# Performance work log

Measured on AMD Instinct MI355X. Metric: run time of the kernel, lower is better.

## Reference

```python
import jax, jax.numpy as jnp
import numpy as np

D, M, N = 1024, 16, 16384
H = D // M  # head dim = 64
C = 10.0    # tanh logit clipping


def setup_inputs() -> dict:
    key = jax.random.key(0)
    kb, kq, km, k1, k2, k3, k4 = jax.random.split(key, 7)
    def xavier(k, shape):
        # torch xavier_uniform: fan_in = prod(shape[1:]), fan_out = shape[0]*prod(shape[2:])
        fan_in = int(np.prod(shape[1:]))
        fan_out = shape[0] * int(np.prod(shape[2:]))
        bound = float(np.sqrt(6.0 / (fan_in + fan_out)))
        return jax.random.uniform(k, shape, jnp.float32, -bound, bound)
    return {
        "b": jax.random.normal(kb, (N, D), jnp.float32),
        "q_s_bar": jax.random.normal(kq, (D,), jnp.float32),
        "mask": jax.random.randint(km, (N,), 0, 2).astype(bool),
        "W_k_bar": xavier(k1, (M, H, D)),
        "W_v_bar": xavier(k2, (M, H, D)),
        "W_k": xavier(k3, (D, D)),
        "W_q": xavier(k4, (D, D)),
    }


def reference(b, q_s_bar, mask, W_k_bar, W_v_bar, W_k, W_q):
    # k_bar, v_bar: (N, M, H)  == matmul(W, b.t()).permute(2,0,1)
    k_bar = jnp.einsum('mhd,nd->nmh', W_k_bar, b)
    v_bar = jnp.einsum('mhd,nd->nmh', W_v_bar, b)
    k = b @ W_k.T                      # (N, D) == matmul(W_k, b.t()).t()
    q = q_s_bar.reshape(M, H)          # (M, H)
    # c_bar: (N, M, M) == matmul(k_bar, q.T) / sqrt(h)
    c_bar = jnp.einsum('nmh,gh->nmg', k_bar, q) / np.float32(np.sqrt(H))
    scores = jnp.where(mask[:, None, None], c_bar, -jnp.inf)
    attn = jax.nn.softmax(scores, axis=0)          # softmax over N
    # (N,M,M) @ (N,M,H) batched -> (N,M,H); view(N,-1).sum(0) -> (D,)
    q_s = jnp.einsum('nmg,ngh->nmh', attn, v_bar).reshape(N, D).sum(0)
    c = (k @ (W_q @ q_s)) / np.float32(np.sqrt(D))  # (N,)
    c = C * jnp.tanh(c)
    return jnp.where(mask, c, -jnp.inf)
```

## Files before the change

### kernel.cpp

```cpp
#include <hip/hip_runtime.h>
#include <math.h>
#include <float.h>

#define NN 16384
#define DD 1024
#define MM 16
#define HH 64
#define MG 256

typedef __attribute__((ext_vector_type(8))) short bh8;
typedef __attribute__((ext_vector_type(4))) float f32x4;

__device__ inline float bf2f(unsigned short u) {
    union { unsigned int i; float f; } v;
    v.i = ((unsigned int)u) << 16;
    return v.f;
}

__device__ inline unsigned short f2bf(float f) {
    union { float f; unsigned int i; } v;
    v.f = f;
    unsigned int r = v.i + 0x7FFFu + ((v.i >> 16) & 1u);
    return (unsigned short)(r >> 16);
}

__device__ inline float ld1(const void* p, long i, int isf) {
    return isf ? ((const float*)p)[i] : bf2f(((const unsigned short*)p)[i]);
}

__device__ inline float4 ld4(const void* p, long i, int isf) {
    if (isf) return *(const float4*)((const float*)p + i);
    ushort4 u = *(const ushort4*)((const unsigned short*)p + i);
    return make_float4(bf2f(u.x), bf2f(u.y), bf2f(u.z), bf2f(u.w));
}

__device__ inline bool get_mask(const unsigned char* mp, int n, int flag) {
    return flag ? (mp[n] != 0) : (mp[4 * n] != 0);
}

__device__ inline void gl_lds16(const void* g, void* l) {
    __builtin_amdgcn_global_load_lds(
        (const __attribute__((address_space(1))) unsigned int*)g,
        (__attribute__((address_space(3))) unsigned int*)l, 16, 0, 0);
}

__global__ void detect(const unsigned char* __restrict__ mp,
                       const unsigned char* __restrict__ bb, int* flags,
                       float* __restrict__ u) {
    int i = blockIdx.x * 256 + threadIdx.x;
    if (i < DD) u[i] = 0.f;
    int v1 = ((i & 3) != 0 && mp[i] != 0) ? 1 : 0;
    unsigned char c = bb[4 * i + 1];
    bool expish = (c == 0x00) || (c == 0x80) || (c >= 0x30 && c <= 0x47) ||
                  (c >= 0xB0 && c <= 0xC7);
    int v2 = expish ? 0 : 1;
    unsigned long long b1 = __ballot(v1);
    unsigned long long b2 = __ballot(v2);
    if ((threadIdx.x & 63) == 0) {
        if (b1) atomicOr(&flags[0], 1);
        if (b2) atomicOr(&flags[1], 1);
    }
}

__global__ void fold_k(const void* __restrict__ Wkb, const void* __restrict__ qsb,
                       unsigned short* __restrict__ Abf, const int* __restrict__ flags) {
    __shared__ float q[DD];
    int isf = flags[1];
    int m = blockIdx.x;
    int d = blockIdx.y * 128 + threadIdx.x;
    for (int i = threadIdx.x; i < DD; i += 128) q[i] = ld1(qsb, i, isf);
    __syncthreads();
    float acc[MM];
#pragma unroll
    for (int g = 0; g < MM; g++) acc[g] = 0.f;
    for (int h = 0; h < HH; h++) {
        float w = ld1(Wkb, (long)(m * HH + h) * DD + d, isf);
#pragma unroll
        for (int g = 0; g < MM; g++) acc[g] += w * q[g * HH + h];
    }
#pragma unroll
    for (int g = 0; g < MM; g++)
        Abf[(long)(m * MM + g) * DD + d] = f2bf(acc[g] * 0.125f);
}

__global__ void cvt_b(const void* __restrict__ bB, unsigned short* __restrict__ bbf,
                      unsigned short* __restrict__ bT, const int* __restrict__ flags) {
    __shared__ unsigned short tl[64 * 72];
    int isf = flags[1];
    int bn = blockIdx.x, bd = blockIdx.y;
    int t = threadIdx.x;
    int i0 = t >> 4, jg = t & 15;
#pragma unroll
    for (int it = 0; it < 4; ++it) {
        int i = i0 + it * 16;
        long gidx = (long)(bn * 64 + i) * DD + bd * 64 + jg * 4;
        ushort4 o;
        if (isf) {
            float4 v = *(const float4*)((const float*)bB + gidx);
            o.x = f2bf(v.x); o.y = f2bf(v.y); o.z = f2bf(v.z); o.w = f2bf(v.w);
        } else {
            o = *(const ushort4*)((const unsigned short*)bB + gidx);
        }
        *(ushort4*)&bbf[gidx] = o;
        *(ushort4*)&tl[i * 72 + jg * 4] = o;
    }
    __syncthreads();
    int p = t >> 2, g = t & 3;
#pragma unroll
    for (int k = 0; k < 4; ++k) {
        int nl = g * 4 + k * 16;
        ushort4 o;
        o.x = tl[(nl + 0) * 72 + p];
        o.y = tl[(nl + 1) * 72 + p];
        o.z = tl[(nl + 2) * 72 + p];
        o.w = tl[(nl + 3) * 72 + p];
        *(ushort4*)&bT[(long)(bd * 64 + p) * NN + bn * 64 + nl] = o;
    }
}

__global__ __launch_bounds__(256) void gemm_b_mfma(
    const unsigned short* __restrict__ Abf, const unsigned short* __restrict__ bbf,
    const unsigned char* __restrict__ mp, const int* __restrict__ flags,
    unsigned short* __restrict__ Cb) {
    __shared__ __align__(16) unsigned short As[128 * 64];
    __shared__ __align__(16) unsigned short Bs[64 * 64];
    int m0 = blockIdx.x * 128, n0 = blockIdx.y * 64;
    int t = threadIdx.x;
    int lane = t & 63, w = t >> 6;
    int wm = w >> 1, wn = w & 1;
    int r = lane & 15, q = lane >> 4;
    f32x4 acc[4][2] = {};
    for (int k0 = 0; k0 < DD; k0 += 64) {
#pragma unroll
        for (int i = 0; i < 4; i++) {
            int L = (i * 4 + w) * 64 + lane;
            int row = L >> 3, c = (L & 7) ^ (row & 7);
            gl_lds16(&Abf[(long)(m0 + row) * DD + k0 + c * 8], &As[(i * 4 + w) * 512]);
        }
#pragma unroll
        for (int i = 0; i < 2; i++) {
            int L = (i * 4 + w) * 64 + lane;
            int row = L >> 3, c = (L & 7) ^ (row & 7);
            gl_lds16(&bbf[(long)(n0 + row) * DD + k0 + c * 8], &Bs[(i * 4 + w) * 512]);
        }
        __syncthreads();
#pragma unroll
        for (int h = 0; h < 2; h++) {
            bh8 af[4], bfr[2];
#pragma unroll
            for (int fi = 0; fi < 4; fi++) {
                int row = wm * 64 + fi * 16 + r;
                int ck = (h * 4 + q) ^ (row & 7);
                af[fi] = *(const bh8*)&As[row * 64 + ck * 8];
            }
#pragma unroll
            for (int fj = 0; fj < 2; fj++) {
                int row = wn * 32 + fj * 16 + r;
                int ck = (h * 4 + q) ^ (row & 7);
                bfr[fj] = *(const bh8*)&Bs[row * 64 + ck * 8];
            }
#pragma unroll
            for (int fi = 0; fi < 4; fi++)
#pragma unroll
                for (int fj = 0; fj < 2; fj++)
                    acc[fi][fj] = __builtin_amdgcn_mfma_f32_16x16x32_bf16(
                        af[fi], bfr[fj], acc[fi][fj], 0, 0, 0);
        }
        __syncthreads();
    }
    int mflag = flags[0];
#pragma unroll
    for (int fj = 0; fj < 2; fj++) {
        int gn = n0 + wn * 32 + fj * 16 + r;
        float nb = get_mask(mp, gn, mflag) ? 0.f : -INFINITY;
#pragma unroll
        for (int fi = 0; fi < 4; fi++)
#pragma unroll
            for (int reg = 0; reg < 4; reg++) {
                int gm = m0 + wm * 64 + fi * 16 + q * 4 + reg;
                Cb[(long)gm * NN + gn] = f2bf(acc[fi][fj][reg] + nb);
            }
    }
}

__global__ void softmax_part(const unsigned short* __restrict__ Cb,
                             float* __restrict__ sws) {
    __shared__ float red[256];
    int mg = blockIdx.x, z = blockIdx.y, t = threadIdx.x;
    bh8 v8 = *(const bh8*)&Cb[(long)mg * NN + z * 2048 + t * 8];
    float x[8];
#pragma unroll
    for (int j = 0; j < 8; j++) x[j] = bf2f((unsigned short)v8[j]);
    float mx = x[0];
#pragma unroll
    for (int j = 1; j < 8; j++) mx = fmaxf(mx, x[j]);
    red[t] = mx;
    __syncthreads();
    for (int s = 128; s; s >>= 1) {
        if (t < s) red[t] = fmaxf(red[t], red[t + s]);
        __syncthreads();
    }
    mx = red[0];
    __syncthreads();
    float sm = 0.f;
#pragma unroll
    for (int j = 0; j < 8; j++) sm += expf(x[j] - mx);
    red[t] = sm;
    __syncthreads();
    for (int s = 128; s; s >>= 1) {
        if (t < s) red[t] += red[t + s];
        __syncthreads();
    }
    if (t == 0) {
        sws[(mg * 8 + z) * 2] = mx;
        sws[(mg * 8 + z) * 2 + 1] = red[0];
    }
}

__global__ void softmax_norm(const unsigned short* __restrict__ Cb,
                             const float* __restrict__ sws,
                             unsigned short* __restrict__ P) {
    int mg = blockIdx.x, z = blockIdx.y, t = threadIdx.x;
    float mx = -INFINITY;
#pragma unroll
    for (int z2 = 0; z2 < 8; z2++) mx = fmaxf(mx, sws[(mg * 8 + z2) * 2]);
    float S = 0.f;
#pragma unroll
    for (int z2 = 0; z2 < 8; z2++) {
        float pm = sws[(mg * 8 + z2) * 2], ps = sws[(mg * 8 + z2) * 2 + 1];
        if (pm > -INFINITY) S += ps * expf(pm - mx);
    }
    float inv = 1.0f / S;
    long i = (long)mg * NN + z * 2048 + t * 8;
    bh8 v8 = *(const bh8*)&Cb[i];
    bh8 o;
#pragma unroll
    for (int j = 0; j < 8; j++)
        o[j] = (short)f2bf(expf(bf2f((unsigned short)v8[j]) - mx) * inv);
    *(bh8*)&P[i] = o;
}

__global__ __launch_bounds__(256) void gemm_d_mfma(
    const unsigned short* __restrict__ P, const unsigned short* __restrict__ bT,
    unsigned short* __restrict__ Tpart) {
    __shared__ __align__(16) unsigned short As[128 * 64];
    __shared__ __align__(16) unsigned short Bs[64 * 64];
    int m0 = blockIdx.x * 128, d0 = blockIdx.y * 64;
    long kbase = (long)blockIdx.z * 1024;
    unsigned short* Cg = Tpart + (long)blockIdx.z * (MG * DD);
    int t = threadIdx.x;
    int lane = t & 63, w = t >> 6;
    int wm = w >> 1, wn = w & 1;
    int r = lane & 15, q = lane >> 4;
    f32x4 acc[4][2] = {};
    for (int k0 = 0; k0 < 1024; k0 += 64) {
#pragma unroll
        for (int i = 0; i < 4; i++) {
            int L = (i * 4 + w) * 64 + lane;
            int row = L >> 3, c = (L & 7) ^ (row & 7);
            gl_lds16(&P[(long)(m0 + row) * NN + kbase + k0 + c * 8], &As[(i * 4 + w) * 512]);
        }
#pragma unroll
        for (int i = 0; i < 2; i++) {
            int L = (i * 4 + w) * 64 + lane;
            int row = L >> 3, c = (L & 7) ^ (row & 7);
            gl_lds16(&bT[(long)(d0 + row) * NN + kbase + k0 + c * 8], &Bs[(i * 4 + w) * 512]);
        }
        __syncthreads();
#pragma unroll
        for (int h = 0; h < 2; h++) {
            bh8 af[4], bfr[2];
#pragma unroll
            for (int fi = 0; fi < 4; fi++) {
                int row = wm * 64 + fi * 16 + r;
                int ck = (h * 4 + q) ^ (row & 7);
                af[fi] = *(const bh8*)&As[row * 64 + ck * 8];
            }
#pragma unroll
            for (int fj = 0; fj < 2; fj++) {
                int row = wn * 32 + fj * 16 + r;
                int ck = (h * 4 + q) ^ (row & 7);
                bfr[fj] = *(const bh8*)&Bs[row * 64 + ck * 8];
            }
#pragma unroll
            for (int fi = 0; fi < 4; fi++)
#pragma unroll
                for (int fj = 0; fj < 2; fj++)
                    acc[fi][fj] = __builtin_amdgcn_mfma_f32_16x16x32_bf16(
                        af[fi], bfr[fj], acc[fi][fj], 0, 0, 0);
        }
        __syncthreads();
    }
#pragma unroll
    for (int fi = 0; fi < 4; fi++)
#pragma unroll
        for (int fj = 0; fj < 2; fj++)
#pragma unroll
            for (int reg = 0; reg < 4; reg++) {
                int gm = m0 + wm * 64 + fi * 16 + q * 4 + reg;
                int gd = d0 + wn * 32 + fj * 16 + r;
                Cg[(long)gm * DD + gd] = f2bf(acc[fi][fj][reg]);
            }
}

__global__ void reduce_T(const unsigned short* __restrict__ Tpart, float* __restrict__ T) {
    long i = (long)(blockIdx.x * 256 + threadIdx.x) * 8;
    float s[8] = {};
#pragma unroll
    for (int c = 0; c < 16; c++) {
        bh8 v = *(const bh8*)&Tpart[(long)c * (MG * DD) + i];
#pragma unroll
        for (int j = 0; j < 8; j++) s[j] += bf2f((unsigned short)v[j]);
    }
    *(float4*)&T[i] = make_float4(s[0], s[1], s[2], s[3]);
    *(float4*)&T[i + 4] = make_float4(s[4], s[5], s[6], s[7]);
}

__global__ void fold_v(const void* __restrict__ Wvb, const float* __restrict__ T,
                       float* __restrict__ qs, const int* __restrict__ flags) {
    int isf = flags[1];
    int w = threadIdx.x >> 6, lane = threadIdx.x & 63;
    int o = blockIdx.x * 4 + w;
    int m = o >> 6, h = o & 63;
    float s = 0.f;
    for (int g = 0; g < MM; g++) {
        const float* Trow = T + (long)(m * MM + g) * DD;
        long wbase = (long)(g * HH + h) * DD;
#pragma unroll
        for (int k = 0; k < 4; k++) {
            int d = lane * 4 + k * 256;
            float4 tv = *(const float4*)&Trow[d];
            float4 wv = ld4(Wvb, wbase + d, isf);
            s += wv.x * tv.x + wv.y * tv.y + wv.z * tv.z + wv.w * tv.w;
        }
    }
    for (int off = 32; off; off >>= 1) s += __shfl_down(s, off, 64);
    if (lane == 0) qs[o] = s;
}

__global__ void matvec_rows(const void* __restrict__ W, const float* __restrict__ x,
                            float* __restrict__ y, const int* __restrict__ flags) {
    int isf = flags[1];
    int lane = threadIdx.x & 63;
    int r = blockIdx.x * 4 + (threadIdx.x >> 6);
    long base = (long)r * DD;
    float s = 0.f;
#pragma unroll
    for (int k = 0; k < 4; k++) {
        int j = lane * 4 + k * 256;
        float4 wv = ld4(W, base + j, isf);
        float4 xv = *(const float4*)&x[j];
        s += wv.x * xv.x + wv.y * xv.y + wv.z * xv.z + wv.w * xv.w;
    }
    for (int off = 32; off; off >>= 1) s += __shfl_down(s, off, 64);
    if (lane == 0) y[r] = s;
}

__global__ void matvec_col(const void* __restrict__ Wk, const float* __restrict__ w1,
                           float* __restrict__ u, const int* __restrict__ flags) {
    __shared__ float xs[16];
    int isf = flags[1];
    int d = blockIdx.x * 256 + threadIdx.x;
    int i0 = blockIdx.y * 16;
    if (threadIdx.x < 16) xs[threadIdx.x] = w1[i0 + threadIdx.x];
    __syncthreads();
    float s = 0.f;
#pragma unroll
    for (int ii = 0; ii < 16; ii++) s += ld1(Wk, (long)(i0 + ii) * DD + d, isf) * xs[ii];
    atomicAdd(&u[d], s);
}

__global__ void final_k(const unsigned short* __restrict__ bbf, const float* __restrict__ u,
                        const unsigned char* __restrict__ mp, const int* __restrict__ flags,
                        void* __restrict__ out) {
    int mflag = flags[0];
    int isf = flags[1];
    int n = blockIdx.x * 4 + (threadIdx.x >> 6);
    int lane = threadIdx.x & 63;
    const unsigned short* row = bbf + (long)n * DD;
    float s = 0.f;
#pragma unroll
    for (int k = 0; k < 4; k++) {
        int j = lane * 4 + k * 256;
        ushort4 v = *(const ushort4*)&row[j];
        float4 uu = *(const float4*)&u[j];
        s += bf2f(v.x) * uu.x + bf2f(v.y) * uu.y + bf2f(v.z) * uu.z + bf2f(v.w) * uu.w;
    }
    for (int off = 32; off; off >>= 1) s += __shfl_down(s, off, 64);
    if (lane == 0) {
        float c = 10.f * tanhf(s * (1.0f / 32.0f));
        bool mk = get_mask(mp, n, mflag);
        if (isf) {
            union { unsigned int i; float f; } vv;
            vv.i = mk ? (((unsigned int)f2bf(c)) << 16) : 0xFF7F0000u;
            ((float*)out)[n] = vv.f;
        } else {
            ((unsigned short*)out)[n] = mk ? f2bf(c) : (unsigned short)0xFF7F;
        }
    }
}

extern "C" void kernel_launch(void* const* d_in, const int* in_sizes, int n_in,
                              void* d_out, int out_size, void* d_ws, size_t ws_size,
                              hipStream_t stream) {
    const void* b = d_in[0];
    const void* qsb = d_in[1];
    const unsigned char* mp = (const unsigned char*)d_in[2];
    const void* Wkb = d_in[3];
    const void* Wvb = d_in[4];
    const void* Wk = d_in[5];
    const void* Wq = d_in[6];

    char* ws = (char*)d_ws;
    unsigned short* bbf = (unsigned short*)(ws);
    unsigned short* bT = (unsigned short*)(ws + (32u << 20));
    unsigned short* Cb = (unsigned short*)(ws + (64u << 20));
    unsigned short* Tpart = (unsigned short*)(ws + (72u << 20));
    unsigned short* P = (unsigned short*)(ws + (80u << 20));
    unsigned short* Abf = (unsigned short*)(ws + (88u << 20));
    float* T = (float*)(ws + (89u << 20));
    float* small = (float*)(ws + (90u << 20));
    float* qs = small;
    float* w1 = qs + 1024;
    float* u = w1 + 1024;
    float* sws = u + 1024;
    int* flags = (int*)(sws + 4096);

    hipMemsetAsync(flags, 0, 2 * sizeof(int), stream);

    detect<<<64, 256, 0, stream>>>(mp, (const unsigned char*)b, flags, u);
    fold_k<<<dim3(16, 8), 128, 0, stream>>>(Wkb, qsb, Abf, flags);
    cvt_b<<<dim3(256, 16), 256, 0, stream>>>(b, bbf, bT, flags);
    gemm_b_mfma<<<dim3(2, 256), 256, 0, stream>>>(Abf, bbf, mp, flags, Cb);
    softmax_part<<<dim3(256, 8), 256, 0, stream>>>(Cb, sws);
    softmax_norm<<<dim3(256, 8), 256, 0, stream>>>(Cb, sws, P);
    gemm_d_mfma<<<dim3(2, 16, 16), 256, 0, stream>>>(P, bT, Tpart);
    reduce_T<<<128, 256, 0, stream>>>(Tpart, T);
    fold_v<<<256, 256, 0, stream>>>(Wvb, T, qs, flags);
    matvec_rows<<<256, 256, 0, stream>>>(Wq, qs, w1, flags);
    matvec_col<<<dim3(4, 64), 256, 0, stream>>>(Wk, w1, u, flags);
    final_k<<<4096, 256, 0, stream>>>(bbf, u, mp, flags, d_out);
}
```

Baseline: 220.9 us.

## Fuse softmax passes, atomically reduce split-K output, restructure b conversion

The two-pass softmax (partial stats plus normalize) becomes one kernel per row that keeps the whole row in registers and reduces with wave shuffles. The split-K partials in gemm_d and the separate reduce_T kernel are replaced by fp32 atomicAdd into T, which is now zeroed in the detect kernel. cvt_b is restructured so each block handles 32 rows across all 1024 columns, with software-prefetched loads and a double-buffered LDS transpose. Together these remove kernel launches and the bf16 partial-buffer traffic, at the cost of atomic contention and a nondeterministic summation order.

```diff
diff --git a/kernel.cpp b/kernel.cpp
--- a/kernel.cpp
+++ b/kernel.cpp
@@ -46,9 +46,12 @@
 
 __global__ void detect(const unsigned char* __restrict__ mp,
                        const unsigned char* __restrict__ bb, int* flags,
-                       float* __restrict__ u) {
+                       float* __restrict__ u, float* __restrict__ T) {
     int i = blockIdx.x * 256 + threadIdx.x;
     if (i < DD) u[i] = 0.f;
+    float4 z = make_float4(0.f, 0.f, 0.f, 0.f);
+#pragma unroll
+    for (int j = 0; j < 4; j++) *(float4*)&T[(j * 16384 + i) * 4] = z;
     int v1 = ((i & 3) != 0 && mp[i] != 0) ? 1 : 0;
     unsigned char c = bb[4 * i + 1];
     bool expish = (c == 0x00) || (c == 0x80) || (c >= 0x30 && c <= 0x47) ||
@@ -83,38 +86,56 @@
         Abf[(long)(m * MM + g) * DD + d] = f2bf(acc[g] * 0.125f);
 }
 
-__global__ void cvt_b(const void* __restrict__ bB, unsigned short* __restrict__ bbf,
-                      unsigned short* __restrict__ bT, const int* __restrict__ flags) {
-    __shared__ unsigned short tl[64 * 72];
-    int isf = flags[1];
-    int bn = blockIdx.x, bd = blockIdx.y;
-    int t = threadIdx.x;
-    int i0 = t >> 4, jg = t & 15;
-#pragma unroll
-    for (int it = 0; it < 4; ++it) {
-        int i = i0 + it * 16;
-        long gidx = (long)(bn * 64 + i) * DD + bd * 64 + jg * 4;
-        ushort4 o;
+__global__ __launch_bounds__(256) void cvt_b(const void* __restrict__ bB,
+                                             unsigned short* __restrict__ bbf,
+                                             unsigned short* __restrict__ bT,
+                                             const int* __restrict__ flags) {
+    __shared__ unsigned short tl[2][32 * 68];
+    const int isf = flags[1];
+    const int t = threadIdx.x;
+    const int n0 = blockIdx.x * 32;
+    const int r = t >> 3, c8 = (t & 7) * 8;
+    const int dT = t >> 2, ch = t & 3;
+    const long gbase = (long)(n0 + r) * DD + c8;
+
+    float cur[8], nxt[8];
+    auto LOAD = [&](float* dst, int dt) {
         if (isf) {
-            float4 v = *(const float4*)((const float*)bB + gidx);
-            o.x = f2bf(v.x); o.y = f2bf(v.y); o.z = f2bf(v.z); o.w = f2bf(v.w);
+            float4 v0 = *(const float4*)((const float*)bB + gbase + dt * 64);
+            float4 v1 = *(const float4*)((const float*)bB + gbase + dt * 64 + 4);
+            dst[0] = v0.x; dst[1] = v0.y; dst[2] = v0.z; dst[3] = v0.w;
+            dst[4] = v1.x; dst[5] = v1.y; dst[6] = v1.z; dst[7] = v1.w;
         } else {
-            o = *(const ushort4*)((const unsigned short*)bB + gidx);
-        }
-        *(ushort4*)&bbf[gidx] = o;
-        *(ushort4*)&tl[i * 72 + jg * 4] = o;
-    }
-    __syncthreads();
-    int p = t >> 2, g = t & 3;
-#pragma unroll
-    for (int k = 0; k < 4; ++k) {
-        int nl = g * 4 + k * 16;
-        ushort4 o;
-        o.x = tl[(nl + 0) * 72 + p];
-        o.y = tl[(nl + 1) * 72 + p];
-        o.z = tl[(nl + 2) * 72 + p];
-        o.w = tl[(nl + 3) * 72 + p];
-        *(ushort4*)&bT[(long)(bd * 64 + p) * NN + bn * 64 + nl] = o;
+            bh8 v = *(const bh8*)((const unsigned short*)bB + gbase + dt * 64);
+#pragma unroll
+            for (int j = 0; j < 8; j++) dst[j] = bf2f((unsigned short)v[j]);
+        }
+    };
+
+    LOAD(cur, 0);
+#pragma unroll
+    for (int dt = 0; dt < 16; dt++) {
+        if (dt < 15) LOAD(nxt, dt + 1);
+        bh8 o;
+#pragma unroll
+        for (int j = 0; j < 8; j++) o[j] = (short)f2bf(cur[j]);
+        *(bh8*)&bbf[gbase + dt * 64] = o;
+        unsigned short* row = &tl[dt & 1][r * 68 + c8];
+        ushort4 lo, hi;
+        lo.x = (unsigned short)o[0]; lo.y = (unsigned short)o[1];
+        lo.z = (unsigned short)o[2]; lo.w = (unsigned short)o[3];
+        hi.x = (unsigned short)o[4]; hi.y = (unsigned short)o[5];
+        hi.z = (unsigned short)o[6]; hi.w = (unsigned short)o[7];
+        *(ushort4*)row = lo;
+        *(ushort4*)(row + 4) = hi;
+        __syncthreads();
+        bh8 y;
+#pragma unroll
+        for (int k = 0; k < 8; k++)
+            y[k] = (short)tl[dt & 1][(ch * 8 + k) * 68 + dT];
+        *(bh8*)&bT[(long)(dt * 64 + dT) * NN + n0 + ch * 8] = y;
+#pragma unroll
+        for (int j = 0; j < 8; j++) cur[j] = nxt[j];
     }
 }
 
@@ -183,71 +204,53 @@
     }
 }
 
-__global__ void softmax_part(const unsigned short* __restrict__ Cb,
-                             float* __restrict__ sws) {
-    __shared__ float red[256];
-    int mg = blockIdx.x, z = blockIdx.y, t = threadIdx.x;
-    bh8 v8 = *(const bh8*)&Cb[(long)mg * NN + z * 2048 + t * 8];
-    float x[8];
-#pragma unroll
-    for (int j = 0; j < 8; j++) x[j] = bf2f((unsigned short)v8[j]);
-    float mx = x[0];
-#pragma unroll
-    for (int j = 1; j < 8; j++) mx = fmaxf(mx, x[j]);
-    red[t] = mx;
+__global__ __launch_bounds__(256) void softmax_f(const unsigned short* __restrict__ Cb,
+                                                 unsigned short* __restrict__ P) {
+    __shared__ float red[8];
+    int mg = blockIdx.x, t = threadIdx.x;
+    long base = (long)mg * NN;
+    bh8 v[8];
+#pragma unroll
+    for (int j = 0; j < 8; j++) v[j] = *(const bh8*)&Cb[base + (j * 256 + t) * 8];
+    float mx = -INFINITY;
+#pragma unroll
+    for (int j = 0; j < 8; j++)
+#pragma unroll
+        for (int e = 0; e < 8; e++) mx = fmaxf(mx, bf2f((unsigned short)v[j][e]));
+#pragma unroll
+    for (int off = 32; off; off >>= 1) mx = fmaxf(mx, __shfl_xor(mx, off, 64));
+    if ((t & 63) == 0) red[t >> 6] = mx;
     __syncthreads();
-    for (int s = 128; s; s >>= 1) {
-        if (t < s) red[t] = fmaxf(red[t], red[t + s]);
-        __syncthreads();
-    }
-    mx = red[0];
+    mx = fmaxf(fmaxf(red[0], red[1]), fmaxf(red[2], red[3]));
+    float mxs = (mx == -INFINITY) ? 0.f : mx;
+    float sm = 0.f;
+#pragma unroll
+    for (int j = 0; j < 8; j++)
+#pragma unroll
+        for (int e = 0; e < 8; e++) sm += expf(bf2f((unsigned short)v[j][e]) - mxs);
+#pragma unroll
+    for (int off = 32; off; off >>= 1) sm += __shfl_xor(sm, off, 64);
+    if ((t & 63) == 0) red[4 + (t >> 6)] = sm;
     __syncthreads();
-    float sm = 0.f;
-#pragma unroll
-    for (int j = 0; j < 8; j++) sm += expf(x[j] - mx);
-    red[t] = sm;
-    __syncthreads();
-    for (int s = 128; s; s >>= 1) {
-        if (t < s) red[t] += red[t + s];
-        __syncthreads();
-    }
-    if (t == 0) {
-        sws[(mg * 8 + z) * 2] = mx;
-        sws[(mg * 8 + z) * 2 + 1] = red[0];
-    }
-}
-
-__global__ void softmax_norm(const unsigned short* __restrict__ Cb,
-                             const float* __restrict__ sws,
-                             unsigned short* __restrict__ P) {
-    int mg = blockIdx.x, z = blockIdx.y, t = threadIdx.x;
-    float mx = -INFINITY;
-#pragma unroll
-    for (int z2 = 0; z2 < 8; z2++) mx = fmaxf(mx, sws[(mg * 8 + z2) * 2]);
-    float S = 0.f;
-#pragma unroll
-    for (int z2 = 0; z2 < 8; z2++) {
-        float pm = sws[(mg * 8 + z2) * 2], ps = sws[(mg * 8 + z2) * 2 + 1];
-        if (pm > -INFINITY) S += ps * expf(pm - mx);
-    }
-    float inv = 1.0f / S;
-    long i = (long)mg * NN + z * 2048 + t * 8;
-    bh8 v8 = *(const bh8*)&Cb[i];
-    bh8 o;
-#pragma unroll
-    for (int j = 0; j < 8; j++)
-        o[j] = (short)f2bf(expf(bf2f((unsigned short)v8[j]) - mx) * inv);
-    *(bh8*)&P[i] = o;
+    sm = red[4] + red[5] + red[6] + red[7];
+    float inv = (sm > 0.f) ? 1.0f / sm : 0.f;
+#pragma unroll
+    for (int j = 0; j < 8; j++) {
+        bh8 o;
+#pragma unroll
+        for (int e = 0; e < 8; e++)
+            o[e] = (short)f2bf(expf(bf2f((unsigned short)v[j][e]) - mxs) * inv);
+        *(bh8*)&P[base + (j * 256 + t) * 8] = o;
+    }
 }
 
 __global__ __launch_bounds__(256) void gemm_d_mfma(
     const unsigned short* __restrict__ P, const unsigned short* __restrict__ bT,
-    unsigned short* __restrict__ Tpart) {
+    float* __restrict__ T) {
     __shared__ __align__(16) unsigned short As[128 * 64];
     __shared__ __align__(16) unsigned short Bs[64 * 64];
     int m0 = blockIdx.x * 128, d0 = blockIdx.y * 64;
     long kbase = (long)blockIdx.z * 1024;
-    unsigned short* Cg = Tpart + (long)blockIdx.z * (MG * DD);
     int t = threadIdx.x;
     int lane = t & 63, w = t >> 6;
     int wm = w >> 1, wn = w & 1;
@@ -299,21 +302,8 @@
             for (int reg = 0; reg < 4; reg++) {
                 int gm = m0 + wm * 64 + fi * 16 + q * 4 + reg;
                 int gd = d0 + wn * 32 + fj * 16 + r;
-                Cg[(long)gm * DD + gd] = f2bf(acc[fi][fj][reg]);
-            }
-}
-
-__global__ void reduce_T(const unsigned short* __restrict__ Tpart, float* __restrict__ T) {
-    long i = (long)(blockIdx.x * 256 + threadIdx.x) * 8;
-    float s[8] = {};
-#pragma unroll
-    for (int c = 0; c < 16; c++) {
-        bh8 v = *(const bh8*)&Tpart[(long)c * (MG * DD) + i];
-#pragma unroll
-        for (int j = 0; j < 8; j++) s[j] += bf2f((unsigned short)v[j]);
-    }
-    *(float4*)&T[i] = make_float4(s[0], s[1], s[2], s[3]);
-    *(float4*)&T[i + 4] = make_float4(s[4], s[5], s[6], s[7]);
+                atomicAdd(&T[(long)gm * DD + gd], acc[fi][fj][reg]);
+            }
 }
 
 __global__ void fold_v(const void* __restrict__ Wvb, const float* __restrict__ T,
@@ -415,7 +405,6 @@
     unsigned short* bbf = (unsigned short*)(ws);
     unsigned short* bT = (unsigned short*)(ws + (32u << 20));
     unsigned short* Cb = (unsigned short*)(ws + (64u << 20));
-    unsigned short* Tpart = (unsigned short*)(ws + (72u << 20));
     unsigned short* P = (unsigned short*)(ws + (80u << 20));
     unsigned short* Abf = (unsigned short*)(ws + (88u << 20));
     float* T = (float*)(ws + (89u << 20));
@@ -423,19 +412,16 @@
     float* qs = small;
     float* w1 = qs + 1024;
     float* u = w1 + 1024;
-    float* sws = u + 1024;
-    int* flags = (int*)(sws + 4096);
+    int* flags = (int*)(u + 1024);
 
     hipMemsetAsync(flags, 0, 2 * sizeof(int), stream);
 
-    detect<<<64, 256, 0, stream>>>(mp, (const unsigned char*)b, flags, u);
+    detect<<<64, 256, 0, stream>>>(mp, (const unsigned char*)b, flags, u, T);
     fold_k<<<dim3(16, 8), 128, 0, stream>>>(Wkb, qsb, Abf, flags);
-    cvt_b<<<dim3(256, 16), 256, 0, stream>>>(b, bbf, bT, flags);
+    cvt_b<<<512, 256, 0, stream>>>(b, bbf, bT, flags);
     gemm_b_mfma<<<dim3(2, 256), 256, 0, stream>>>(Abf, bbf, mp, flags, Cb);
-    softmax_part<<<dim3(256, 8), 256, 0, stream>>>(Cb, sws);
-    softmax_norm<<<dim3(256, 8), 256, 0, stream>>>(Cb, sws, P);
-    gemm_d_mfma<<<dim3(2, 16, 16), 256, 0, stream>>>(P, bT, Tpart);
-    reduce_T<<<128, 256, 0, stream>>>(Tpart, T);
+    softmax_f<<<256, 256, 0, stream>>>(Cb, P);
+    gemm_d_mfma<<<dim3(2, 16, 16), 256, 0, stream>>>(P, bT, T);
     fold_v<<<256, 256, 0, stream>>>(Wvb, T, qs, flags);
     matvec_rows<<<256, 256, 0, stream>>>(Wq, qs, w1, flags);
     matvec_col<<<dim3(4, 64), 256, 0, stream>>>(Wk, w1, u, flags);
```

Measured after the change: 231.9 us. 1.05x slower.
